# Kernel tuning notes

Hardware: AMD Instinct MI355X
Metric: run time of the kernel (lower is better)

The kernel has to match this reference:

```python
import jax, jax.numpy as jnp
import numpy as np

WIN = 7
NUM_HEADS = 3


def _relative_position_index():
    # Faithful to the TF code: tf.meshgrid defaults to 'xy' indexing.
    ch = jnp.arange(WIN)
    cw = jnp.arange(WIN)
    coords = jnp.stack(jnp.meshgrid(ch, cw, indexing='xy'))          # [2, 7, 7]
    flat = coords.reshape(2, WIN * WIN)                               # [2, 49]
    rel = flat[:, :, None] - flat[:, None, :]                         # [2, 49, 49]
    rel = jnp.transpose(rel, (1, 2, 0))                               # [49, 49, 2]
    rel = rel.at[:, :, 0].add(WIN - 1)
    rel = rel.at[:, :, 1].add(WIN - 1)
    rel = rel.at[:, :, 0].multiply(2 * WIN - 1)
    return jnp.sum(rel, axis=-1).astype(jnp.int32)                    # [49, 49]


def setup_inputs() -> dict:
    key = jax.random.key(0)
    k1, k2, k3, k4 = jax.random.split(key, 4)
    B_, N, C = 16384, 49, 96
    nW = 1024
    x = jax.random.normal(k1, (B_, N, C), dtype=jnp.float32)
    mask = jnp.zeros((nW, N, N), dtype=jnp.float32)  # 0 = attend
    qkv_w = jax.random.normal(k2, (C, 3 * C), dtype=jnp.float32) * 0.02
    qkv_b = jnp.zeros((3 * C,), dtype=jnp.float32)
    proj_w = jax.random.normal(k3, (C, C), dtype=jnp.float32) * 0.02
    proj_b = jnp.zeros((C,), dtype=jnp.float32)
    n_rel = (2 * WIN - 1) * (2 * WIN - 1)  # 169
    bias_table = jax.random.normal(k4, (n_rel, NUM_HEADS), dtype=jnp.float32) * 0.02
    rel_idx = _relative_position_index()
    return {"x": x, "mask": mask, "qkv_w": qkv_w, "qkv_b": qkv_b,
            "proj_w": proj_w, "proj_b": proj_b, "bias_table": bias_table,
            "rel_idx": rel_idx}


def reference(x, mask, qkv_w, qkv_b, proj_w, proj_b, bias_table, rel_idx):
    B_, N, C = x.shape
    H = NUM_HEADS
    hd = C // H
    scale = hd ** -0.5
    # qkv projection: [B_, N, 3C] -> [3, B_, H, N, hd]
    qkv = (x @ qkv_w + qkv_b).reshape(B_, N, 3, H, hd)
    qkv = jnp.transpose(qkv, (2, 0, 3, 1, 4))
    q, k, v = qkv[0] * scale, qkv[1], qkv[2]
    attn = jnp.einsum('bhnd,bhmd->bhnm', q, k)                        # [B_, H, N, N]
    # relative position bias gather: [169, H] -> [H, N, N]
    rpb = bias_table[rel_idx.reshape(-1)].reshape(N, N, H)
    rpb = jnp.transpose(rpb, (2, 0, 1))
    attn = attn + rpb[None]
    # window mask add: [nW, N, N] broadcast over batch and heads
    nW = mask.shape[0]
    attn = attn.reshape(B_ // nW, nW, H, N, N) + mask[None, :, None]
    attn = attn.reshape(B_, H, N, N)
    # NOTE: the original code applies softmax TWICE (once in the branch,
    # once unconditionally). We replicate that faithfully.
    attn = jax.nn.softmax(attn, axis=-1)
    attn = jax.nn.softmax(attn, axis=-1)
    out = jnp.einsum('bhnm,bhmd->bhnd', attn, v)                      # [B_, H, N, hd]
    out = jnp.transpose(out, (0, 2, 1, 3)).reshape(B_, N, C)
    return out @ proj_w + proj_b
```

## Files before the change

### kernel.cpp

```cpp
#include <hip/hip_runtime.h>
#include <hip/hip_bf16.h>
#include <math.h>

typedef __bf16 bf16_t;
typedef bf16_t bf16x8 __attribute__((ext_vector_type(8)));
typedef bf16_t bf16x4 __attribute__((ext_vector_type(4)));
typedef float  f32x4  __attribute__((ext_vector_type(4)));
typedef unsigned int u32;

#define NTOK 49
#define CDIM 96
#define NH   3
#define NWIN 1024

__device__ __forceinline__ f32x4 mfma16(bf16x8 a, bf16x8 b, f32x4 c) {
    return __builtin_amdgcn_mfma_f32_16x16x32_bf16(a, b, c, 0, 0, 0);
}

__device__ __forceinline__ u32 pk2(float lo, float hi) {
    union { bf16_t h[2]; u32 u; } t;
    t.h[0] = (bf16_t)lo; t.h[1] = (bf16_t)hi;
    return t.u;
}

__global__ void prep_kernel(const float* __restrict__ qkv_w,
                            const float* __restrict__ proj_w,
                            const float* __restrict__ bias_table,
                            const int*   __restrict__ rel_idx,
                            bf16_t* __restrict__ wqT,
                            bf16_t* __restrict__ wpT,
                            float*  __restrict__ rpbf)
{
    const int stride = gridDim.x * blockDim.x;
    const int i0 = blockIdx.x * blockDim.x + threadIdx.x;
    for (int e = i0; e < 288 * 96; e += stride) {
        int n = e / 96, k = e - n * 96;
        wqT[e] = (bf16_t)qkv_w[k * 288 + n];
    }
    for (int e = i0; e < 96 * 96; e += stride) {
        int n = e / 96, k = e - n * 96;
        wpT[e] = (bf16_t)proj_w[k * 96 + n];
    }
    for (int e = i0; e < 3 * 64 * 64; e += stride) {
        int h = e >> 12, r = (e >> 6) & 63, c = e & 63;
        float v;
        if (c >= NTOK)      v = -1e9f;
        else if (r >= NTOK) v = 0.0f;
        else                v = bias_table[rel_idx[r * NTOK + c] * NH + h];
        rpbf[e] = v;
    }
}

__global__ void __launch_bounds__(192, 3)
wattn_kernel(const float* __restrict__ x,
             const float* __restrict__ mask,
             const float* __restrict__ qkv_b,
             const float* __restrict__ proj_b,
             const bf16_t* __restrict__ wqT,
             const bf16_t* __restrict__ wpT,
             const float*  __restrict__ rpbf,
             float* __restrict__ out)
{
    __shared__ alignas(16) char smem[40448];
    bf16_t (*xs)[104] = reinterpret_cast<bf16_t(*)[104]>(smem);
    bf16_t (*vT)[72]  = reinterpret_cast<bf16_t(*)[72]>(smem);
    bf16_t (*qs)[104] = reinterpret_cast<bf16_t(*)[104]>(smem + 13824);
    bf16_t (*kk)[104] = reinterpret_cast<bf16_t(*)[104]>(smem + 27136);

    const int b    = blockIdx.x;
    const int tid  = threadIdx.x;
    const int w    = tid >> 6;
    const int lane = tid & 63;
    const int r16  = lane & 15;
    const int g    = lane >> 4;
    const int g8   = g << 3;
    const int g4   = g << 2;

    const float scale = 0.17677669529663687f;

    {
        const float* xb = x + (size_t)b * (NTOK * CDIM);
        #pragma unroll
        for (int it = 0; it < 8; ++it) {
            int q4 = tid + it * 192;
            int e  = q4 * 4;
            int r  = e / 96, c = e - r * 96;
            float4 v;
            if (q4 < 1176) v = *reinterpret_cast<const float4*>(xb + e);
            else           v = make_float4(0.f, 0.f, 0.f, 0.f);
            bf16x4 o = { (bf16_t)v.x, (bf16_t)v.y, (bf16_t)v.z, (bf16_t)v.w };
            *reinterpret_cast<bf16x4*>(&xs[r][c]) = o;
        }
    }
    __syncthreads();

    {
        bf16x8 afr[4][3];
        #pragma unroll
        for (int mt = 0; mt < 4; ++mt)
            #pragma unroll
            for (int ks = 0; ks < 3; ++ks)
                afr[mt][ks] = *reinterpret_cast<const bf16x8*>(&xs[mt * 16 + r16][ks * 32 + g8]);

        __syncthreads();

        #pragma unroll
        for (int nt6 = 0; nt6 < 6; ++nt6) {
            const int col = (w * 6 + nt6) * 16 + r16;
            f32x4 acc[4];
            #pragma unroll
            for (int mt = 0; mt < 4; ++mt) acc[mt] = (f32x4){0.f, 0.f, 0.f, 0.f};
            #pragma unroll
            for (int ks = 0; ks < 3; ++ks) {
                bf16x8 bfr = *reinterpret_cast<const bf16x8*>(wqT + col * 96 + ks * 32 + g8);
                #pragma unroll
                for (int mt = 0; mt < 4; ++mt) acc[mt] = mfma16(afr[mt][ks], bfr, acc[mt]);
            }
            const float bias = qkv_b[col];
            #pragma unroll
            for (int mt = 0; mt < 4; ++mt)
                #pragma unroll
                for (int j = 0; j < 4; ++j) {
                    const int row = mt * 16 + g4 + j;
                    const float v = acc[mt][j] + bias;
                    if (w == 0)      qs[row][col]       = (bf16_t)(v * scale);
                    else if (w == 1) kk[row][col - 96]  = (bf16_t)v;
                    else             vT[col - 192][row] = (bf16_t)v;
                }
        }
    }
    __syncthreads();

    const int h = w;
    {
        bf16x8 qa[4], kb[4], vb[2][2];
        #pragma unroll
        for (int t = 0; t < 4; ++t) {
            qa[t] = *reinterpret_cast<const bf16x8*>(&qs[t * 16 + r16][h * 32 + g8]);
            kb[t] = *reinterpret_cast<const bf16x8*>(&kk[t * 16 + r16][h * 32 + g8]);
        }
        #pragma unroll
        for (int dt = 0; dt < 2; ++dt)
            #pragma unroll
            for (int c = 0; c < 2; ++c)
                vb[dt][c] = *reinterpret_cast<const bf16x8*>(&vT[h * 32 + dt * 16 + r16][c * 32 + g8]);

        const float* rpbh = rpbf + h * 4096;
        const float* mrow = mask + (size_t)(b & (NWIN - 1)) * (NTOK * NTOK);
        const int srcA = ((g & 1) << 5) + r16;
        const int srcB = srcA + 16;
        const bool lo = (g < 2);

        #pragma unroll
        for (int nt = 0; nt < 4; ++nt) {
            f32x4 sv[4];
            #pragma unroll
            for (int mt = 0; mt < 4; ++mt) {
                f32x4 z = (f32x4){0.f, 0.f, 0.f, 0.f};
                sv[mt] = mfma16(kb[mt], qa[nt], z);
            }
            const int q = nt * 16 + r16;
            const int rpbase = q << 6;
            const int mbase  = q * NTOK;
            float s[4][4];
            #pragma unroll
            for (int mt = 0; mt < 4; ++mt)
                #pragma unroll
                for (int j = 0; j < 4; ++j) {
                    const int key = mt * 16 + g4 + j;
                    float v = sv[mt][j] + rpbh[rpbase + key];
                    if ((mt < 3 || (j == 0 && g == 0)) && q < NTOK)
                        v += mrow[mbase + key];
                    s[mt][j] = v;
                }

            float mx = -3.0e38f;
            #pragma unroll
            for (int mt = 0; mt < 4; ++mt)
                #pragma unroll
                for (int j = 0; j < 4; ++j) mx = fmaxf(mx, s[mt][j]);
            mx = fmaxf(mx, __shfl_xor(mx, 16));
            mx = fmaxf(mx, __shfl_xor(mx, 32));
            float e1[4][4];
            float sum1 = 0.f;
            #pragma unroll
            for (int mt = 0; mt < 4; ++mt)
                #pragma unroll
                for (int j = 0; j < 4; ++j) {
                    float t = __expf(s[mt][j] - mx);
                    e1[mt][j] = t; sum1 += t;
                }
            sum1 += __shfl_xor(sum1, 16);
            sum1 += __shfl_xor(sum1, 32);
            const float inv1 = __builtin_amdgcn_rcpf(sum1);

            float e2[4][4];
            float sum2 = 0.f;
            #pragma unroll
            for (int mt = 0; mt < 4; ++mt)
                #pragma unroll
                for (int j = 0; j < 4; ++j) {
                    float t = __expf(e1[mt][j] * inv1);
                    e2[mt][j] = t; sum2 += t;
                }
            sum2 += __shfl_xor(sum2, 16);
            sum2 += __shfl_xor(sum2, 32);
            sum2 -= 15.0f;
            const float inv2 = __builtin_amdgcn_rcpf(sum2);

            u32 d01[4], d23[4];
            #pragma unroll
            for (int mt = 0; mt < 4; ++mt) {
                float p0 = e2[mt][0] * inv2, p1 = e2[mt][1] * inv2;
                float p2 = e2[mt][2] * inv2, p3 = e2[mt][3] * inv2;
                if (mt == 3) { p0 = (g == 0) ? p0 : 0.f; p1 = 0.f; p2 = 0.f; p3 = 0.f; }
                d01[mt] = pk2(p0, p1);
                d23[mt] = pk2(p2, p3);
            }
            u32 m0a0 = __shfl(d01[0], srcA), m0a1 = __shfl(d23[0], srcA);
            u32 m0b0 = __shfl(d01[0], srcB), m0b1 = __shfl(d23[0], srcB);
            u32 m1a0 = __shfl(d01[1], srcA), m1a1 = __shfl(d23[1], srcA);
            u32 m1b0 = __shfl(d01[1], srcB), m1b1 = __shfl(d23[1], srcB);
            u32 m2a0 = __shfl(d01[2], srcA), m2a1 = __shfl(d23[2], srcA);
            u32 m2b0 = __shfl(d01[2], srcB), m2b1 = __shfl(d23[2], srcB);
            u32 m3a0 = __shfl(d01[3], srcA), m3a1 = __shfl(d23[3], srcA);
            u32 m3b0 = __shfl(d01[3], srcB), m3b1 = __shfl(d23[3], srcB);

            union U8 { u32 d[4]; bf16x8 v; } ua, ub;
            ua.d[0] = lo ? m0a0 : m1a0;  ua.d[1] = lo ? m0a1 : m1a1;
            ua.d[2] = lo ? m0b0 : m1b0;  ua.d[3] = lo ? m0b1 : m1b1;
            ub.d[0] = lo ? m2a0 : m3a0;  ub.d[1] = lo ? m2a1 : m3a1;
            ub.d[2] = lo ? m2b0 : m3b0;  ub.d[3] = lo ? m2b1 : m3b1;

            #pragma unroll
            for (int dt = 0; dt < 2; ++dt) {
                f32x4 z = (f32x4){0.f, 0.f, 0.f, 0.f};
                f32x4 o = mfma16(ua.v, vb[dt][0], z);
                o = mfma16(ub.v, vb[dt][1], o);
                const int dcol = h * 32 + dt * 16 + r16;
                #pragma unroll
                for (int j = 0; j < 4; ++j)
                    qs[nt * 16 + g4 + j][dcol] = (bf16_t)o[j];
            }
        }
    }
    __syncthreads();

    {
        #pragma unroll
        for (int n2 = 0; n2 < 2; ++n2) {
            const int col = w * 32 + n2 * 16 + r16;
            f32x4 acc[4];
            #pragma unroll
            for (int mt = 0; mt < 4; ++mt) acc[mt] = (f32x4){0.f, 0.f, 0.f, 0.f};
            #pragma unroll
            for (int ks = 0; ks < 3; ++ks) {
                bf16x8 bfr = *reinterpret_cast<const bf16x8*>(wpT + col * 96 + ks * 32 + g8);
                #pragma unroll
                for (int mt = 0; mt < 4; ++mt) {
                    bf16x8 oa = *reinterpret_cast<const bf16x8*>(&qs[mt * 16 + r16][ks * 32 + g8]);
                    acc[mt] = mfma16(oa, bfr, acc[mt]);
                }
            }
            const float pb = proj_b[col];
            #pragma unroll
            for (int mt = 0; mt < 4; ++mt)
                #pragma unroll
                for (int j = 0; j < 4; ++j) {
                    const int row = mt * 16 + g4 + j;
                    if (row < NTOK)
                        out[((size_t)b * NTOK + row) * CDIM + col] = acc[mt][j] + pb;
                }
        }
    }
}

extern "C" void kernel_launch(void* const* d_in, const int* in_sizes, int n_in,
                              void* d_out, int out_size, void* d_ws, size_t ws_size,
                              hipStream_t stream) {
    const float* x          = (const float*)d_in[0];
    const float* mask       = (const float*)d_in[1];
    const float* qkv_w      = (const float*)d_in[2];
    const float* qkv_b      = (const float*)d_in[3];
    const float* proj_w     = (const float*)d_in[4];
    const float* proj_b     = (const float*)d_in[5];
    const float* bias_table = (const float*)d_in[6];
    const int*   rel_idx    = (const int*)d_in[7];
    float* out = (float*)d_out;

    char* ws = (char*)d_ws;
    bf16_t* wqT  = (bf16_t*)(ws);
    bf16_t* wpT  = (bf16_t*)(ws + 55296);
    float*  rpbf = (float*) (ws + 55296 + 18432);

    prep_kernel<<<64, 256, 0, stream>>>(qkv_w, proj_w, bias_table, rel_idx, wqT, wpT, rpbf);

    const int nwin = in_sizes[0] / (NTOK * CDIM);
    wattn_kernel<<<nwin, 192, 0, stream>>>(x, mask, qkv_b, proj_b, wqT, wpT, rpbf, out);
}
```

Baseline: 887.3 us.

## Compute QKV per head in registers via shuffles, shrink LDS, pad mask for vector loads

Each wave now computes its own head's Q, K and V projections directly in MFMA fragment layout and redistributes them with lane shuffles, instead of staging the full Q/K/V in LDS. This cuts shared memory from about 40KB to about 13KB and raises the launch-bounds occupancy hint from 3 to 4 blocks per CU. A prep pass pads the window mask to 64x64 in workspace so the score stage can use float4 loads without per-element bounds checks. The padded-mask path needs a larger workspace and a much bigger prep launch, and the register-held fragments raise register pressure.

Measured after the change: 765.6 us. 13.7% less time.

```diff
diff --git a/kernel.cpp b/kernel.cpp
--- a/kernel.cpp
+++ b/kernel.cpp
@@ -27,9 +27,11 @@
                             const float* __restrict__ proj_w,
                             const float* __restrict__ bias_table,
                             const int*   __restrict__ rel_idx,
+                            const float* __restrict__ mask,
                             bf16_t* __restrict__ wqT,
                             bf16_t* __restrict__ wpT,
-                            float*  __restrict__ rpbf)
+                            float*  __restrict__ rpbf,
+                            float*  __restrict__ maskp)
 {
     const int stride = gridDim.x * blockDim.x;
     const int i0 = blockIdx.x * blockDim.x + threadIdx.x;
@@ -49,11 +51,19 @@
         else                v = bias_table[rel_idx[r * NTOK + c] * NH + h];
         rpbf[e] = v;
     }
-}
-
-__global__ void __launch_bounds__(192, 3)
+    if (maskp) {
+        for (int e = i0; e < NWIN * 64 * 64; e += stride) {
+            int widx = e >> 12, r = (e >> 6) & 63, c = e & 63;
+            maskp[e] = (r < NTOK && c < NTOK) ? mask[widx * (NTOK * NTOK) + r * NTOK + c] : 0.0f;
+        }
+    }
+}
+
+template <bool MP>
+__global__ void __launch_bounds__(192, 4)
 wattn_kernel(const float* __restrict__ x,
              const float* __restrict__ mask,
+             const float* __restrict__ maskp,
              const float* __restrict__ qkv_b,
              const float* __restrict__ proj_b,
              const bf16_t* __restrict__ wqT,
@@ -61,22 +71,22 @@
              const float*  __restrict__ rpbf,
              float* __restrict__ out)
 {
-    __shared__ alignas(16) char smem[40448];
-    bf16_t (*xs)[104] = reinterpret_cast<bf16_t(*)[104]>(smem);
-    bf16_t (*vT)[72]  = reinterpret_cast<bf16_t(*)[72]>(smem);
-    bf16_t (*qs)[104] = reinterpret_cast<bf16_t(*)[104]>(smem + 13824);
-    bf16_t (*kk)[104] = reinterpret_cast<bf16_t(*)[104]>(smem + 27136);
+    __shared__ alignas(16) bf16_t xs[64][104];
 
     const int b    = blockIdx.x;
     const int tid  = threadIdx.x;
-    const int w    = tid >> 6;
+    const int h    = tid >> 6;
     const int lane = tid & 63;
     const int r16  = lane & 15;
     const int g    = lane >> 4;
     const int g8   = g << 3;
     const int g4   = g << 2;
-
     const float scale = 0.17677669529663687f;
+
+    const int srcA = ((g & 1) << 5) + r16;
+    const int srcB = srcA + 16;
+    const bool hi  = (g >= 2);
+    const bool lo  = !hi;
 
     {
         const float* xb = x + (size_t)b * (NTOK * CDIM);
@@ -94,62 +104,92 @@
     }
     __syncthreads();
 
+    bf16x8 qa[4], kb[4], vb[2][2];
     {
-        bf16x8 afr[4][3];
+        u32 d01[2][4], d23[2][4];
         #pragma unroll
-        for (int mt = 0; mt < 4; ++mt)
-            #pragma unroll
-            for (int ks = 0; ks < 3; ++ks)
-                afr[mt][ks] = *reinterpret_cast<const bf16x8*>(&xs[mt * 16 + r16][ks * 32 + g8]);
-
-        __syncthreads();
-
-        #pragma unroll
-        for (int nt6 = 0; nt6 < 6; ++nt6) {
-            const int col = (w * 6 + nt6) * 16 + r16;
-            f32x4 acc[4];
-            #pragma unroll
-            for (int mt = 0; mt < 4; ++mt) acc[mt] = (f32x4){0.f, 0.f, 0.f, 0.f};
-            #pragma unroll
-            for (int ks = 0; ks < 3; ++ks) {
-                bf16x8 bfr = *reinterpret_cast<const bf16x8*>(wqT + col * 96 + ks * 32 + g8);
-                #pragma unroll
-                for (int mt = 0; mt < 4; ++mt) acc[mt] = mfma16(afr[mt][ks], bfr, acc[mt]);
-            }
-            const float bias = qkv_b[col];
-            #pragma unroll
-            for (int mt = 0; mt < 4; ++mt)
-                #pragma unroll
-                for (int j = 0; j < 4; ++j) {
-                    const int row = mt * 16 + g4 + j;
-                    const float v = acc[mt][j] + bias;
-                    if (w == 0)      qs[row][col]       = (bf16_t)(v * scale);
-                    else if (w == 1) kk[row][col - 96]  = (bf16_t)v;
-                    else             vT[col - 192][row] = (bf16_t)v;
+        for (int sec = 0; sec < 2; ++sec) {
+            const int base = sec * 96 + h * 32;
+            #pragma unroll
+            for (int dt = 0; dt < 2; ++dt) {
+                bf16x8 wf[3];
+                #pragma unroll
+                for (int ks = 0; ks < 3; ++ks)
+                    wf[ks] = *reinterpret_cast<const bf16x8*>(wqT + (base + dt * 16 + r16) * 96 + ks * 32 + g8);
+                float4 b4 = *reinterpret_cast<const float4*>(qkv_b + base + dt * 16 + g4);
+                #pragma unroll
+                for (int t = 0; t < 4; ++t) {
+                    f32x4 acc = (f32x4){0.f, 0.f, 0.f, 0.f};
+                    #pragma unroll
+                    for (int ks = 0; ks < 3; ++ks)
+                        acc = mfma16(wf[ks], *reinterpret_cast<const bf16x8*>(&xs[t * 16 + r16][ks * 32 + g8]), acc);
+                    if (sec == 0) {
+                        d01[dt][t] = pk2((acc[0] + b4.x) * scale, (acc[1] + b4.y) * scale);
+                        d23[dt][t] = pk2((acc[2] + b4.z) * scale, (acc[3] + b4.w) * scale);
+                    } else {
+                        d01[dt][t] = pk2(acc[0] + b4.x, acc[1] + b4.y);
+                        d23[dt][t] = pk2(acc[2] + b4.z, acc[3] + b4.w);
+                    }
+                }
+            }
+            #pragma unroll
+            for (int t = 0; t < 4; ++t) {
+                u32 a0, b0;
+                union U8 { u32 d[4]; bf16x8 v; } u;
+                a0 = __shfl(d01[0][t], srcA); b0 = __shfl(d01[1][t], srcA); u.d[0] = hi ? b0 : a0;
+                a0 = __shfl(d23[0][t], srcA); b0 = __shfl(d23[1][t], srcA); u.d[1] = hi ? b0 : a0;
+                a0 = __shfl(d01[0][t], srcB); b0 = __shfl(d01[1][t], srcB); u.d[2] = hi ? b0 : a0;
+                a0 = __shfl(d23[0][t], srcB); b0 = __shfl(d23[1][t], srcB); u.d[3] = hi ? b0 : a0;
+                if (sec == 0) qa[t] = u.v; else kb[t] = u.v;
+            }
+        }
+        u32 vd01[4][2], vd23[4][2];
+        {
+            bf16x8 vwf[2][3];
+            float vbias[2];
+            #pragma unroll
+            for (int dt = 0; dt < 2; ++dt) {
+                #pragma unroll
+                for (int ks = 0; ks < 3; ++ks)
+                    vwf[dt][ks] = *reinterpret_cast<const bf16x8*>(wqT + (192 + h * 32 + dt * 16 + r16) * 96 + ks * 32 + g8);
+                vbias[dt] = qkv_b[192 + h * 32 + dt * 16 + r16];
+            }
+            #pragma unroll
+            for (int mt = 0; mt < 4; ++mt) {
+                bf16x8 af[3];
+                #pragma unroll
+                for (int ks = 0; ks < 3; ++ks)
+                    af[ks] = *reinterpret_cast<const bf16x8*>(&xs[mt * 16 + r16][ks * 32 + g8]);
+                #pragma unroll
+                for (int dt = 0; dt < 2; ++dt) {
+                    f32x4 acc = (f32x4){0.f, 0.f, 0.f, 0.f};
+                    #pragma unroll
+                    for (int ks = 0; ks < 3; ++ks)
+                        acc = mfma16(af[ks], vwf[dt][ks], acc);
+                    vd01[mt][dt] = pk2(acc[0] + vbias[dt], acc[1] + vbias[dt]);
+                    vd23[mt][dt] = pk2(acc[2] + vbias[dt], acc[3] + vbias[dt]);
+                }
+            }
+            #pragma unroll
+            for (int dt = 0; dt < 2; ++dt)
+                #pragma unroll
+                for (int c = 0; c < 2; ++c) {
+                    u32 a0, b0;
+                    union U8 { u32 d[4]; bf16x8 v; } u;
+                    a0 = __shfl(vd01[2 * c][dt], srcA); b0 = __shfl(vd01[2 * c + 1][dt], srcA); u.d[0] = hi ? b0 : a0;
+                    a0 = __shfl(vd23[2 * c][dt], srcA); b0 = __shfl(vd23[2 * c + 1][dt], srcA); u.d[1] = hi ? b0 : a0;
+                    a0 = __shfl(vd01[2 * c][dt], srcB); b0 = __shfl(vd01[2 * c + 1][dt], srcB); u.d[2] = hi ? b0 : a0;
+                    a0 = __shfl(vd23[2 * c][dt], srcB); b0 = __shfl(vd23[2 * c + 1][dt], srcB); u.d[3] = hi ? b0 : a0;
+                    vb[dt][c] = u.v;
                 }
         }
     }
     __syncthreads();
 
-    const int h = w;
     {
-        bf16x8 qa[4], kb[4], vb[2][2];
-        #pragma unroll
-        for (int t = 0; t < 4; ++t) {
-            qa[t] = *reinterpret_cast<const bf16x8*>(&qs[t * 16 + r16][h * 32 + g8]);
-            kb[t] = *reinterpret_cast<const bf16x8*>(&kk[t * 16 + r16][h * 32 + g8]);
-        }
-        #pragma unroll
-        for (int dt = 0; dt < 2; ++dt)
-            #pragma unroll
-            for (int c = 0; c < 2; ++c)
-                vb[dt][c] = *reinterpret_cast<const bf16x8*>(&vT[h * 32 + dt * 16 + r16][c * 32 + g8]);
-
-        const float* rpbh = rpbf + h * 4096;
-        const float* mrow = mask + (size_t)(b & (NWIN - 1)) * (NTOK * NTOK);
-        const int srcA = ((g & 1) << 5) + r16;
-        const int srcB = srcA + 16;
-        const bool lo = (g < 2);
+        const float* rpbh   = rpbf + h * 4096;
+        const float* maskph = MP ? (maskp + (size_t)(b & (NWIN - 1)) * 4096) : nullptr;
+        const float* mrow   = MP ? nullptr : (mask + (size_t)(b & (NWIN - 1)) * (NTOK * NTOK));
 
         #pragma unroll
         for (int nt = 0; nt < 4; ++nt) {
@@ -159,20 +199,31 @@
                 f32x4 z = (f32x4){0.f, 0.f, 0.f, 0.f};
                 sv[mt] = mfma16(kb[mt], qa[nt], z);
             }
-            const int q = nt * 16 + r16;
-            const int rpbase = q << 6;
-            const int mbase  = q * NTOK;
+            const int qi = nt * 16 + r16;
             float s[4][4];
-            #pragma unroll
-            for (int mt = 0; mt < 4; ++mt)
-                #pragma unroll
-                for (int j = 0; j < 4; ++j) {
-                    const int key = mt * 16 + g4 + j;
-                    float v = sv[mt][j] + rpbh[rpbase + key];
-                    if ((mt < 3 || (j == 0 && g == 0)) && q < NTOK)
-                        v += mrow[mbase + key];
-                    s[mt][j] = v;
-                }
+            if (MP) {
+                #pragma unroll
+                for (int mt = 0; mt < 4; ++mt) {
+                    float4 r4 = *reinterpret_cast<const float4*>(rpbh + (qi << 6) + mt * 16 + g4);
+                    float4 m4 = *reinterpret_cast<const float4*>(maskph + (qi << 6) + mt * 16 + g4);
+                    s[mt][0] = sv[mt][0] + r4.x + m4.x;
+                    s[mt][1] = sv[mt][1] + r4.y + m4.y;
+                    s[mt][2] = sv[mt][2] + r4.z + m4.z;
+                    s[mt][3] = sv[mt][3] + r4.w + m4.w;
+                }
+            } else {
+                const int mbase = qi * NTOK;
+                #pragma unroll
+                for (int mt = 0; mt < 4; ++mt)
+                    #pragma unroll
+                    for (int j = 0; j < 4; ++j) {
+                        const int key = mt * 16 + g4 + j;
+                        float v = sv[mt][j] + rpbh[(qi << 6) + key];
+                        if ((mt < 3 || (j == 0 && g == 0)) && qi < NTOK)
+                            v += mrow[mbase + key];
+                        s[mt][j] = v;
+                    }
+            }
 
             float mx = -3.0e38f;
             #pragma unroll
@@ -240,7 +291,7 @@
                 const int dcol = h * 32 + dt * 16 + r16;
                 #pragma unroll
                 for (int j = 0; j < 4; ++j)
-                    qs[nt * 16 + g4 + j][dcol] = (bf16_t)o[j];
+                    xs[nt * 16 + g4 + j][dcol] = (bf16_t)o[j];
             }
         }
     }
@@ -249,7 +300,7 @@
     {
         #pragma unroll
         for (int n2 = 0; n2 < 2; ++n2) {
-            const int col = w * 32 + n2 * 16 + r16;
+            const int col = h * 32 + n2 * 16 + r16;
             f32x4 acc[4];
             #pragma unroll
             for (int mt = 0; mt < 4; ++mt) acc[mt] = (f32x4){0.f, 0.f, 0.f, 0.f};
@@ -258,7 +309,7 @@
                 bf16x8 bfr = *reinterpret_cast<const bf16x8*>(wpT + col * 96 + ks * 32 + g8);
                 #pragma unroll
                 for (int mt = 0; mt < 4; ++mt) {
-                    bf16x8 oa = *reinterpret_cast<const bf16x8*>(&qs[mt * 16 + r16][ks * 32 + g8]);
+                    bf16x8 oa = *reinterpret_cast<const bf16x8*>(&xs[mt * 16 + r16][ks * 32 + g8]);
                     acc[mt] = mfma16(oa, bfr, acc[mt]);
                 }
             }
@@ -292,9 +343,19 @@
     bf16_t* wqT  = (bf16_t*)(ws);
     bf16_t* wpT  = (bf16_t*)(ws + 55296);
     float*  rpbf = (float*) (ws + 55296 + 18432);
-
-    prep_kernel<<<64, 256, 0, stream>>>(qkv_w, proj_w, bias_table, rel_idx, wqT, wpT, rpbf);
+    const size_t maskp_off = 122880;
+    const size_t maskp_sz  = (size_t)NWIN * 64 * 64 * 4;
+    const bool mp = ws_size >= maskp_off + maskp_sz;
+    float* maskp = mp ? (float*)(ws + maskp_off) : nullptr;
+
+    prep_kernel<<<mp ? 2048 : 64, 256, 0, stream>>>(qkv_w, proj_w, bias_table, rel_idx,
+                                                    mask, wqT, wpT, rpbf, maskp);
 
     const int nwin = in_sizes[0] / (NTOK * CDIM);
-    wattn_kernel<<<nwin, 192, 0, stream>>>(x, mask, qkv_b, proj_b, wqT, wpT, rpbf, out);
-}
+    if (mp)
+        wattn_kernel<true><<<nwin, 192, 0, stream>>>(x, mask, maskp, qkv_b, proj_b,
+                                                     wqT, wpT, rpbf, out);
+    else
+        wattn_kernel<false><<<nwin, 192, 0, stream>>>(x, mask, maskp, qkv_b, proj_b,
+                                                      wqT, wpT, rpbf, out);
+}
```
